# Kernel optimization log

Hardware: AMD Instinct MI355X
Metric: run time of the kernel (lower is better)

Reference implementation:

```python
import jax, jax.numpy as jnp
import numpy as np
import math

A, B, C, D = 32, 32, 8, 16
K, STRIDE, PAD, ITERS = 3, 1, 1, 3
KK = K * K
KKA = KK * A


def squash(s, axis=-1):
    mag_sq = jnp.sum(s ** 2, axis=axis, keepdims=True)
    mag = jnp.sqrt(mag_sq)
    return mag_sq / (1.0 + mag_sq) * (s / mag)


def setup_inputs() -> dict:
    key = jax.random.key(0)
    k1, k2 = jax.random.split(key)
    pose = jax.random.normal(k1, (4, A * C, 14, 14), dtype=jnp.float32)
    # kaiming_uniform_ on (KKA, B*D, C): fan_in = (B*D)*C = 4096, bound = sqrt(6/fan_in)
    bound = math.sqrt(6.0 / (B * D * C))
    W = jax.random.uniform(k2, (KKA, B * D, C), dtype=jnp.float32, minval=-bound, maxval=bound)
    return {"pose": pose, "W": W}


def reference(pose, W):
    b, _, h, w = pose.shape
    # F.unfold equivalent: (b, A*C*kk, oh, ow), channel-major then kernel-position ordering
    patches = jax.lax.conv_general_dilated_patches(
        pose, (K, K), (STRIDE, STRIDE), [(PAD, PAD), (PAD, PAD)])
    l = patches.shape[2] * patches.shape[3]
    x = patches.reshape(b, A, C, KK, l)
    x = jnp.transpose(x, (0, 4, 3, 1, 2)).reshape(b, l, KKA, C)  # (b,l,kkA,C)
    # pose_out[b,l,k,:] = W[k] @ x[b,l,k]  -> (b,l,kkA,B*D)
    pose_out = jnp.einsum('kpc,blkc->blkp', W, x).reshape(b, l, KKA, B, D)
    logits = jnp.zeros((b, l, KKA, B, 1), dtype=pose.dtype)
    v = None
    for _ in range(ITERS):
        c = jax.nn.softmax(logits, axis=3)                      # over B capsules
        s = jnp.sum(c * pose_out, axis=2, keepdims=True)        # (b,l,1,B,D)
        v = squash(s)
        logits = logits + jnp.sum(v * pose_out, axis=-1, keepdims=True)
    v = v[:, :, 0]                                              # (b,l,B,D)
    v = jnp.transpose(v.reshape(b, l, B * D), (0, 2, 1))        # (b,B*D,l)
    oh = math.isqrt(l)
    return v.reshape(b, B * D, oh, oh)
```

## Files before the change

kernel.cpp:

```cpp
#include <hip/hip_runtime.h>
#include <stdint.h>

#define NSITES 784
#define LSZ    196
#define HWD    14
#define KKA_   288
#define BD_    512
#define NRG    6
#define ROWS_PER_BLK 48
#define ROWS_PER_WAVE 12
#define SITES_PER_BLK 4

#define WH_OFF    0
#define XH_OFF    2359296
#define PART_OFF  5971968
#define VBUF_OFF  15605760
#define WS_NEED   17211392

typedef _Float16 h2 __attribute__((ext_vector_type(2)));

#define PIN8(p) asm volatile("" : "+v"(p[0]),"+v"(p[1]),"+v"(p[2]),"+v"(p[3]), \
                                  "+v"(p[4]),"+v"(p[5]),"+v"(p[6]),"+v"(p[7]))

__device__ __forceinline__ float dot8(const uint4 wv, const uint4 xv) {
    h2 w0 = __builtin_bit_cast(h2, wv.x), w1 = __builtin_bit_cast(h2, wv.y),
       w2 = __builtin_bit_cast(h2, wv.z), w3 = __builtin_bit_cast(h2, wv.w);
    h2 x0 = __builtin_bit_cast(h2, xv.x), x1 = __builtin_bit_cast(h2, xv.y),
       x2 = __builtin_bit_cast(h2, xv.z), x3 = __builtin_bit_cast(h2, xv.w);
#if __has_builtin(__builtin_amdgcn_fdot2)
    float acc = __builtin_amdgcn_fdot2(w0, x0, 0.f, false);
    acc = __builtin_amdgcn_fdot2(w1, x1, acc, false);
    acc = __builtin_amdgcn_fdot2(w2, x2, acc, false);
    acc = __builtin_amdgcn_fdot2(w3, x3, acc, false);
    return acc;
#else
    float acc = (float)w0.x*(float)x0.x + (float)w0.y*(float)x0.y
              + (float)w1.x*(float)x1.x + (float)w1.y*(float)x1.y
              + (float)w2.x*(float)x2.x + (float)w2.y*(float)x2.y
              + (float)w3.x*(float)x3.x + (float)w3.y*(float)x3.y;
    return acc;
#endif
}

__global__ __launch_bounds__(256) void k_prep(
    const float* __restrict__ pose, const float* __restrict__ W,
    uint4* __restrict__ Wh, uint4* __restrict__ xh)
{
    const int t  = threadIdx.x;
    const int bx = blockIdx.x;
    if (bx < NSITES) {
        const int site = bx;
        const int b = site / LSZ;
        const int l = site - b * LSZ;
        const int oh = l / HWD, ow = l - oh * HWD;
        for (int kk = t; kk < KKA_; kk += 256) {
            const int p = kk >> 5, a = kk & 31;
            const int ky = p / 3 - 1, kx = p % 3 - 1;
            const int y = oh + ky, x = ow + kx;
            const bool inb = (y >= 0 && y < HWD && x >= 0 && x < HWD);
            const float* pp = pose + ((size_t)b * 256 + a * 8) * LSZ
                            + (inb ? (y * HWD + x) : 0);
            uint32_t uo[4];
            #pragma unroll
            for (int cp = 0; cp < 4; ++cp) {
                const float f0 = inb ? pp[(2*cp)   * LSZ] : 0.f;
                const float f1 = inb ? pp[(2*cp+1) * LSZ] : 0.f;
                h2 hh; hh.x = (_Float16)f0; hh.y = (_Float16)f1;
                uo[cp] = __builtin_bit_cast(uint32_t, hh);
            }
            uint4 o; o.x = uo[0]; o.y = uo[1]; o.z = uo[2]; o.w = uo[3];
            xh[(size_t)site * KKA_ + kk] = o;
        }
    } else {
        const int wb = bx - NSITES;
        const int kk = wb * 4 + (t >> 6);
        const int ln = t & 63;
        const float* Wr = W + (size_t)kk * (BD_ * 8);
        #pragma unroll
        for (int u = 0; u < 8; ++u) {
            const int p = ln * 8 + u;
            const float4 fa = *(const float4*)(Wr + p * 8);
            const float4 fb = *(const float4*)(Wr + p * 8 + 4);
            uint32_t uo[4];
            h2 h0; h0.x=(_Float16)fa.x; h0.y=(_Float16)fa.y; uo[0]=__builtin_bit_cast(uint32_t,h0);
            h2 h1; h1.x=(_Float16)fa.z; h1.y=(_Float16)fa.w; uo[1]=__builtin_bit_cast(uint32_t,h1);
            h2 h2v; h2v.x=(_Float16)fb.x; h2v.y=(_Float16)fb.y; uo[2]=__builtin_bit_cast(uint32_t,h2v);
            h2 h3; h3.x=(_Float16)fb.z; h3.y=(_Float16)fb.w; uo[3]=__builtin_bit_cast(uint32_t,h3);
            uint4 o; o.x=uo[0]; o.y=uo[1]; o.z=uo[2]; o.w=uo[3];
            Wh[(size_t)kk * 512 + u * 64 + ln] = o;
        }
    }
}

template<int PASS>
__global__ __launch_bounds__(256, 4) void k_sweep(
    const uint4* __restrict__ Wh, const uint4* __restrict__ xh,
    const float* __restrict__ vbuf, float* __restrict__ partial)
{
    const int t  = threadIdx.x;
    const int w  = t >> 6;
    const int ln = t & 63;
    const int sg = blockIdx.x;
    const int rg = blockIdx.y;
    const int site0 = sg * SITES_PER_BLK;
    const int kk0 = __builtin_amdgcn_readfirstlane(rg * ROWS_PER_BLK + w);

    float v[SITES_PER_BLK][8];
    if (PASS >= 2) {
        #pragma unroll
        for (int s = 0; s < SITES_PER_BLK; ++s) {
            const float4* vp = (const float4*)(vbuf + (size_t)(site0 + s) * BD_ + ln * 8);
            const float4 a = vp[0], bq = vp[1];
            v[s][0]=a.x;  v[s][1]=a.y;  v[s][2]=a.z;  v[s][3]=a.w;
            v[s][4]=bq.x; v[s][5]=bq.y; v[s][6]=bq.z; v[s][7]=bq.w;
            PIN8(v[s]);
        }
    }

    float sacc[SITES_PER_BLK][8];
    #pragma unroll
    for (int s = 0; s < SITES_PER_BLK; ++s)
        #pragma unroll
        for (int j = 0; j < 8; ++j) sacc[s][j] = 0.f;

    const uint4* Wrow = Wh + (size_t)kk0 * 512;
    const uint4* xrow = xh + kk0;

    #pragma unroll 1
    for (int r = 0; r < ROWS_PER_WAVE; ++r) {
        uint4 wr[8];
        #pragma unroll
        for (int u = 0; u < 8; ++u) wr[u] = Wrow[u * 64 + ln];
        Wrow += 4 * 512;

        #pragma unroll
        for (int s = 0; s < SITES_PER_BLK; ++s) {
            const uint4 xr = xrow[(size_t)(site0 + s) * KKA_];
            float po[8];
            #pragma unroll
            for (int j = 0; j < 8; ++j) po[j] = dot8(wr[j], xr);
            if (PASS == 1) {
                #pragma unroll
                for (int j = 0; j < 8; ++j) sacc[s][j] += po[j];
            } else {
                float up = v[s][0] * po[0];
                #pragma unroll
                for (int j = 1; j < 8; ++j) up += v[s][j] * po[j];
                up += __shfl_xor(up, 1, 64);
                const float e = __expf(up);
                float se = e;
                se += __shfl_xor(se, 2, 64);
                se += __shfl_xor(se, 4, 64);
                se += __shfl_xor(se, 8, 64);
                se += __shfl_xor(se, 16, 64);
                se += __shfl_xor(se, 32, 64);
                const float c = e * __builtin_amdgcn_rcpf(se);
                #pragma unroll
                for (int j = 0; j < 8; ++j) sacc[s][j] += c * po[j];
            }
        }
        xrow += 4;
    }

    __shared__ float red[4 * BD_];
    #pragma unroll
    for (int s = 0; s < SITES_PER_BLK; ++s) {
        if (s) __syncthreads();
        float4 r0, r1;
        r0.x=sacc[s][0]; r0.y=sacc[s][1]; r0.z=sacc[s][2]; r0.w=sacc[s][3];
        r1.x=sacc[s][4]; r1.y=sacc[s][5]; r1.z=sacc[s][6]; r1.w=sacc[s][7];
        *(float4*)&red[w * BD_ + ln * 8]     = r0;
        *(float4*)&red[w * BD_ + ln * 8 + 4] = r1;
        __syncthreads();
        #pragma unroll
        for (int pp = 0; pp < 2; ++pp) {
            const int p = t + pp * 256;
            partial[((size_t)(site0 + s) * NRG + rg) * BD_ + p] =
                red[p] + red[BD_ + p] + red[2*BD_ + p] + red[3*BD_ + p];
        }
    }
}

template<int PASS>
__global__ __launch_bounds__(256) void k_reduce(
    const float* __restrict__ partial, float* __restrict__ vbuf,
    float* __restrict__ out)
{
    const int site = blockIdx.x * 4 + (threadIdx.x >> 6);
    const int ln = threadIdx.x & 63;
    float tv[8] = {0.f,0.f,0.f,0.f,0.f,0.f,0.f,0.f};
    #pragma unroll
    for (int rg = 0; rg < NRG; ++rg) {
        const float4* pp4 = (const float4*)(partial + ((size_t)site * NRG + rg) * BD_ + ln * 8);
        const float4 a = pp4[0], b = pp4[1];
        tv[0]+=a.x; tv[1]+=a.y; tv[2]+=a.z; tv[3]+=a.w;
        tv[4]+=b.x; tv[5]+=b.y; tv[6]+=b.z; tv[7]+=b.w;
    }
    if (PASS == 1) {
        #pragma unroll
        for (int j = 0; j < 8; ++j) tv[j] *= (1.f / 32.f);
    }
    float msq = 0.f;
    #pragma unroll
    for (int j = 0; j < 8; ++j) msq += tv[j] * tv[j];
    msq += __shfl_xor(msq, 1, 64);
    const float fac = sqrtf(msq) / (1.f + msq);
    if (PASS == 1) {
        #pragma unroll
        for (int j = 0; j < 8; ++j) vbuf[(size_t)site * BD_ + ln * 8 + j] = tv[j] * fac;
    } else if (PASS == 2) {
        #pragma unroll
        for (int j = 0; j < 8; ++j) vbuf[(size_t)site * BD_ + ln * 8 + j] += tv[j] * fac;
    } else {
        const int b = site / LSZ;
        const int l = site - b * LSZ;
        float* op = out + (size_t)b * BD_ * LSZ + l;
        #pragma unroll
        for (int j = 0; j < 8; ++j) op[(size_t)(ln * 8 + j) * LSZ] = tv[j] * fac;
    }
}

extern "C" void kernel_launch(void* const* d_in, const int* in_sizes, int n_in,
                              void* d_out, int out_size, void* d_ws, size_t ws_size,
                              hipStream_t stream) {
    const float* pose = (const float*)d_in[0];
    const float* W    = (const float*)d_in[1];
    float* out        = (float*)d_out;

    if (ws_size < (size_t)WS_NEED) return;

    uint8_t* ws = (uint8_t*)d_ws;
    uint4*  Wh     = (uint4*)  (ws + WH_OFF);
    uint4*  xh     = (uint4*)  (ws + XH_OFF);
    float* partial = (float*)  (ws + PART_OFF);
    float* vbuf    = (float*)  (ws + VBUF_OFF);

    k_prep<<<dim3(NSITES + 72), dim3(256), 0, stream>>>(pose, W, Wh, xh);

    const dim3 gs(NSITES / SITES_PER_BLK, NRG);
    k_sweep<1><<<gs, dim3(256), 0, stream>>>(Wh, xh, vbuf, partial);
    k_reduce<1><<<dim3(NSITES / 4), dim3(256), 0, stream>>>(partial, vbuf, out);
    k_sweep<2><<<gs, dim3(256), 0, stream>>>(Wh, xh, vbuf, partial);
    k_reduce<2><<<dim3(NSITES / 4), dim3(256), 0, stream>>>(partial, vbuf, out);
    k_sweep<3><<<gs, dim3(256), 0, stream>>>(Wh, xh, vbuf, partial);
    k_reduce<3><<<dim3(NSITES / 4), dim3(256), 0, stream>>>(partial, vbuf, out);
}
```

Measured before the change: 187.0 us.

## Double-buffer weight row loads and batch softmax shuffles across sites in sweep

The sweep loop now prefetches the next row's fp16 weight vectors into a second register buffer while the current row is computed, unrolling the loop by two. The routing pass batches the dot products, exp and cross-lane shuffle reductions for all four sites so the independent shuffles can interleave, which should hide their latency. Launch bounds drop from 4 to 2 blocks per SM so the extra registers fit, at the cost of fewer resident waves. The final prefetch reads one row past the weight rows, which lands inside the workspace and is never used.

```diff
diff --git a/kernel.cpp b/kernel.cpp
--- a/kernel.cpp
+++ b/kernel.cpp
@@ -84,7 +84,7 @@
             uint32_t uo[4];
             h2 h0; h0.x=(_Float16)fa.x; h0.y=(_Float16)fa.y; uo[0]=__builtin_bit_cast(uint32_t,h0);
             h2 h1; h1.x=(_Float16)fa.z; h1.y=(_Float16)fa.w; uo[1]=__builtin_bit_cast(uint32_t,h1);
-            h2 h2v; h2v.x=(_Float16)fb.x; h2v.y=(_Float16)fb.y; uo[2]=__builtin_bit_cast(uint32_t,h2v);
+            h2 hv; hv.x=(_Float16)fb.x; hv.y=(_Float16)fb.y; uo[2]=__builtin_bit_cast(uint32_t,hv);
             h2 h3; h3.x=(_Float16)fb.z; h3.y=(_Float16)fb.w; uo[3]=__builtin_bit_cast(uint32_t,h3);
             uint4 o; o.x=uo[0]; o.y=uo[1]; o.z=uo[2]; o.w=uo[3];
             Wh[(size_t)kk * 512 + u * 64 + ln] = o;
@@ -93,7 +93,51 @@
 }
 
 template<int PASS>
-__global__ __launch_bounds__(256, 4) void k_sweep(
+__device__ __forceinline__ void row_body(
+    const uint4 wr[8], const uint4* __restrict__ xrow, int site0,
+    const float v[SITES_PER_BLK][8], float sacc[SITES_PER_BLK][8])
+{
+    if (PASS == 1) {
+        #pragma unroll
+        for (int s = 0; s < SITES_PER_BLK; ++s) {
+            const uint4 xr = xrow[(size_t)(site0 + s) * KKA_];
+            #pragma unroll
+            for (int j = 0; j < 8; ++j) sacc[s][j] += dot8(wr[j], xr);
+        }
+    } else {
+        float po[SITES_PER_BLK][8];
+        float up[SITES_PER_BLK];
+        #pragma unroll
+        for (int s = 0; s < SITES_PER_BLK; ++s) {
+            const uint4 xr = xrow[(size_t)(site0 + s) * KKA_];
+            #pragma unroll
+            for (int j = 0; j < 8; ++j) po[s][j] = dot8(wr[j], xr);
+            float u = v[s][0] * po[s][0];
+            #pragma unroll
+            for (int j = 1; j < 8; ++j) u += v[s][j] * po[s][j];
+            up[s] = u;
+        }
+        #pragma unroll
+        for (int s = 0; s < SITES_PER_BLK; ++s) up[s] += __shfl_xor(up[s], 1, 64);
+        float e4[SITES_PER_BLK], se4[SITES_PER_BLK];
+        #pragma unroll
+        for (int s = 0; s < SITES_PER_BLK; ++s) { e4[s] = __expf(up[s]); se4[s] = e4[s]; }
+        #pragma unroll
+        for (int m = 2; m < 64; m <<= 1) {
+            #pragma unroll
+            for (int s = 0; s < SITES_PER_BLK; ++s) se4[s] += __shfl_xor(se4[s], m, 64);
+        }
+        #pragma unroll
+        for (int s = 0; s < SITES_PER_BLK; ++s) {
+            const float c = e4[s] * __builtin_amdgcn_rcpf(se4[s]);
+            #pragma unroll
+            for (int j = 0; j < 8; ++j) sacc[s][j] += c * po[s][j];
+        }
+    }
+}
+
+template<int PASS>
+__global__ __launch_bounds__(256, 2) void k_sweep(
     const uint4* __restrict__ Wh, const uint4* __restrict__ xh,
     const float* __restrict__ vbuf, float* __restrict__ partial)
 {
@@ -126,39 +170,22 @@
     const uint4* Wrow = Wh + (size_t)kk0 * 512;
     const uint4* xrow = xh + kk0;
 
+    uint4 wa[8], wb[8];
+    #pragma unroll
+    for (int u = 0; u < 8; ++u) wa[u] = Wrow[u * 64 + ln];
+    Wrow += 4 * 512;
+
     #pragma unroll 1
-    for (int r = 0; r < ROWS_PER_WAVE; ++r) {
-        uint4 wr[8];
-        #pragma unroll
-        for (int u = 0; u < 8; ++u) wr[u] = Wrow[u * 64 + ln];
+    for (int r = 0; r < ROWS_PER_WAVE; r += 2) {
+        #pragma unroll
+        for (int u = 0; u < 8; ++u) wb[u] = Wrow[u * 64 + ln];
         Wrow += 4 * 512;
-
-        #pragma unroll
-        for (int s = 0; s < SITES_PER_BLK; ++s) {
-            const uint4 xr = xrow[(size_t)(site0 + s) * KKA_];
-            float po[8];
-            #pragma unroll
-            for (int j = 0; j < 8; ++j) po[j] = dot8(wr[j], xr);
-            if (PASS == 1) {
-                #pragma unroll
-                for (int j = 0; j < 8; ++j) sacc[s][j] += po[j];
-            } else {
-                float up = v[s][0] * po[0];
-                #pragma unroll
-                for (int j = 1; j < 8; ++j) up += v[s][j] * po[j];
-                up += __shfl_xor(up, 1, 64);
-                const float e = __expf(up);
-                float se = e;
-                se += __shfl_xor(se, 2, 64);
-                se += __shfl_xor(se, 4, 64);
-                se += __shfl_xor(se, 8, 64);
-                se += __shfl_xor(se, 16, 64);
-                se += __shfl_xor(se, 32, 64);
-                const float c = e * __builtin_amdgcn_rcpf(se);
-                #pragma unroll
-                for (int j = 0; j < 8; ++j) sacc[s][j] += c * po[j];
-            }
-        }
+        row_body<PASS>(wa, xrow, site0, v, sacc);
+        xrow += 4;
+        #pragma unroll
+        for (int u = 0; u < 8; ++u) wa[u] = Wrow[u * 64 + ln];
+        Wrow += 4 * 512;
+        row_body<PASS>(wb, xrow, site0, v, sacc);
         xrow += 4;
     }
 
```

After: 209.1 us. +11.8%, slower.
